# Performance work log

Hardware: AMD Instinct MI355X
Metric: run time of the kernel (lower is better)

The kernel has to match this reference:

```python
import jax, jax.numpy as jnp
import numpy as np

# Lens/CCD constants from the source module
DX = 0.00859375
F = 8.0
OX = 5.5 / 2.0   # CCD_width / 2
OY = 7.7 / 2.0   # CCD_length / 2

B, C, H, W = 4, 3, 1024, 2048


def _make_bn(h, w):
    # bn[i, j] = floor((cos(atan(dx*(j-ox)/f)) - 1) * (i - oy)), as in __init__
    j = np.arange(w, dtype=np.float64)
    i = np.arange(h, dtype=np.float64)
    a0 = np.arctan(DX * (j - OX) / F)
    bn = np.floor((np.cos(a0)[None, :] - 1.0) * (i[:, None] - OY))
    return bn.astype(np.int32)


def setup_inputs() -> dict:
    key = jax.random.key(0)
    k1, k2 = jax.random.split(key)
    x = jax.random.normal(k1, (B, C, H, W), dtype=jnp.float32)
    # Conv2d(3, 3, kernel_size=3, bias=False) weight: (out_c, in_c, kh, kw)
    weight = jax.random.normal(k2, (3, 3, 3, 3), dtype=jnp.float32) * 0.1
    bn = jnp.asarray(_make_bn(H, W))  # int32 distortion LUT, shape (H, W)
    return {"x": x, "weight": weight, "bn": bn}


def reference(x, weight, bn):
    B_, C_, H_, W_ = x.shape
    Hi, Wj = H_ - 2, W_ // 2 - 2  # active region: i+2 < H and j+2 < W//2
    i = jnp.arange(Hi)
    j = jnp.arange(Wj)
    p = jnp.arange(3)  # k // 3 (patch row)
    q = jnp.arange(3)  # k % 3  (patch col)
    # column used for the LUT wraps for j >= 256 (j1 = j % 256)
    j1 = jnp.where(j >= 256, j % 256, j)
    rows = i[:, None] + p[None, :]        # (Hi, 3)
    cols = j1[:, None] + q[None, :]       # (Wj, 3)
    # tb(i, j, p, q) = i + p + bn[i + p, j1 + q]
    bn_sel = bn[rows[:, None, :, None], cols[None, :, None, :]]  # (Hi, Wj, 3, 3)
    R = rows[:, None, :, None] + bn_sel                          # source row indices
    # Faithful quirk from the source: patch column index into input is q (0..2),
    # NOT j + q: matrix1[:, :, p, q] = input[:, :, tb, q]
    gathered = x[:, :, R, q]  # (B, C, Hi, Wj, 3, 3)
    out_act = jnp.einsum('bcijpq,ocpq->boij', gathered, weight)  # per-pixel 3x3 conv
    # guard from the source: only write when i + 2 + bn[i+2, j+2] < H
    mask = (i[:, None] + 2 + bn[i[:, None] + 2, j[None, :] + 2]) < H_
    out_act = out_act * mask.astype(out_act.dtype)
    return jnp.zeros((B_, C_, H_, W_), x.dtype).at[:, :, :Hi, :Wj].set(out_act)
```

## Files before the change

### kernel.cpp

```cpp
#include <hip/hip_runtime.h>


#define HH 1024
#define WW 2048
#define HI 1022
#define WJ 1022

#define VWS_FLOATS (12 * 1024 * 256)

__global__ __launch_bounds__(256) void compute_v_kernel(
    const float* __restrict__ x,
    const float* __restrict__ w,
    const int*   __restrict__ bn,
    float*       __restrict__ ws)
{
    const int i  = blockIdx.x;
    const int jm = threadIdx.x;

    int Rv[3][3];
    #pragma unroll
    for (int p = 0; p < 3; ++p) {
        const int r = i + p;
        const int* bnrow = bn + (size_t)r * WW;
        #pragma unroll
        for (int q = 0; q < 3; ++q) {
            int rv = r + bnrow[jm + q];
            if (rv < 0) rv += HH;
            Rv[p][q] = rv;
        }
    }

    float acc[4][3];
    #pragma unroll
    for (int b = 0; b < 4; ++b)
        #pragma unroll
        for (int o = 0; o < 3; ++o)
            acc[b][o] = 0.f;

    #pragma unroll
    for (int b = 0; b < 4; ++b) {
        #pragma unroll
        for (int c = 0; c < 3; ++c) {
            const float* xbase = x + (size_t)(b * 3 + c) * (HH * WW);
            #pragma unroll
            for (int p = 0; p < 3; ++p) {
                #pragma unroll
                for (int q = 0; q < 3; ++q) {
                    const float xv = xbase[(size_t)Rv[p][q] * WW + q];
                    #pragma unroll
                    for (int o = 0; o < 3; ++o)
                        acc[b][o] += xv * w[(o * 3 + c) * 9 + p * 3 + q];
                }
            }
        }
    }

    #pragma unroll
    for (int b = 0; b < 4; ++b)
        #pragma unroll
        for (int o = 0; o < 3; ++o)
            ws[((size_t)(b * 3 + o) * HH + i) * 256 + jm] = acc[b][o];

    float* mws = ws + VWS_FLOATS;
    const int* bnm = bn + (size_t)(i + 2) * WW;
    #pragma unroll
    for (int k = 0; k < 4; ++k) {
        const int j = jm + 256 * k;
        float m = 0.f;
        if (j < WJ)
            m = ((i + 2) + bnm[j + 2] < HH) ? 1.f : 0.f;
        mws[(size_t)i * 1024 + j] = m;
    }
}

__global__ __launch_bounds__(256) void write_kernel(
    const float* __restrict__ ws,
    float*       __restrict__ out)
{
    const int bi = blockIdx.x;
    const int b  = bi >> 10;
    const int i  = bi & 1023;
    const int j4 = threadIdx.x * 4;

    const float4 z = make_float4(0.f, 0.f, 0.f, 0.f);

    if (i < HI) {
        const float* mrow = ws + VWS_FLOATS + (size_t)i * 1024;
        const float4 mm = *(const float4*)&mrow[j4];
        #pragma unroll
        for (int o = 0; o < 3; ++o) {
            const float* vrow = ws + ((size_t)(b * 3 + o) * HH + i) * 256;
            const float4 vv = *(const float4*)&vrow[j4 & 255];
            float* orow = out + ((size_t)(b * 3 + o) * HH + i) * WW;
            *(float4*)&orow[j4] = make_float4(vv.x * mm.x, vv.y * mm.y,
                                              vv.z * mm.z, vv.w * mm.w);
            *(float4*)&orow[j4 + 1024] = z;
        }
    } else {
        #pragma unroll
        for (int o = 0; o < 3; ++o) {
            float* orow = out + ((size_t)(b * 3 + o) * HH + i) * WW;
            *(float4*)&orow[j4]        = z;
            *(float4*)&orow[j4 + 1024] = z;
        }
    }
}

extern "C" void kernel_launch(void* const* d_in, const int* in_sizes, int n_in,
                              void* d_out, int out_size, void* d_ws, size_t ws_size,
                              hipStream_t stream) {
    const float* x   = (const float*)d_in[0];
    const float* w   = (const float*)d_in[1];
    const int*   bn  = (const int*)d_in[2];
    float*       out = (float*)d_out;
    float*       ws  = (float*)d_ws;

    compute_v_kernel<<<dim3(HI), dim3(256), 0, stream>>>(x, w, bn, ws);
    write_kernel<<<dim3(4096), dim3(256), 0, stream>>>(ws, out);
}
```

Before: 190.4 us.

## Fuse compute and write kernels into one kernel staging values in shared memory

Merges the two-kernel pipeline into a single kernel where each block computes its row's 256 per-column conv values and mask into shared memory, then writes the full output row for all batches and channels directly. This removes the global workspace round-trip and one kernel launch. Each block now does more serial work (12 row stores) and only 1024 blocks are launched instead of 1022 plus 4096, which may reduce store parallelism.

Result: faster. 183.4 us (-3.7%).

```diff
diff --git a/kernel.cpp b/kernel.cpp
--- a/kernel.cpp
+++ b/kernel.cpp
@@ -6,29 +6,19 @@
 #define HI 1022
 #define WJ 1022
 
-#define VWS_FLOATS (12 * 1024 * 256)
-
-__global__ __launch_bounds__(256) void compute_v_kernel(
+__global__ __launch_bounds__(256) void dis_conv_kernel(
     const float* __restrict__ x,
     const float* __restrict__ w,
     const int*   __restrict__ bn,
-    float*       __restrict__ ws)
+    float*       __restrict__ out)
 {
-    const int i  = blockIdx.x;
-    const int jm = threadIdx.x;
+    const int i = blockIdx.x;
+    const int t = threadIdx.x;
 
-    int Rv[3][3];
-    #pragma unroll
-    for (int p = 0; p < 3; ++p) {
-        const int r = i + p;
-        const int* bnrow = bn + (size_t)r * WW;
-        #pragma unroll
-        for (int q = 0; q < 3; ++q) {
-            int rv = r + bnrow[jm + q];
-            if (rv < 0) rv += HH;
-            Rv[p][q] = rv;
-        }
-    }
+    __shared__ __align__(16) float v[12][256];
+    __shared__ __align__(16) float mask_s[1024];
+
+    const bool activeRow = (i < HI);
 
     float acc[4][3];
     #pragma unroll
@@ -37,72 +27,62 @@
         for (int o = 0; o < 3; ++o)
             acc[b][o] = 0.f;
 
-    #pragma unroll
-    for (int b = 0; b < 4; ++b) {
+    if (activeRow) {
+        int Rv[3][3];
         #pragma unroll
-        for (int c = 0; c < 3; ++c) {
-            const float* xbase = x + (size_t)(b * 3 + c) * (HH * WW);
+        for (int p = 0; p < 3; ++p) {
+            const int* bnrow = bn + (size_t)(i + p) * WW;
             #pragma unroll
-            for (int p = 0; p < 3; ++p) {
+            for (int q = 0; q < 3; ++q) {
+                int rv = i + p + bnrow[t + q];
+                if (rv < 0) rv += HH;
+                Rv[p][q] = rv;
+            }
+        }
+        #pragma unroll
+        for (int b = 0; b < 4; ++b) {
+            #pragma unroll
+            for (int c = 0; c < 3; ++c) {
+                const float* xbase = x + (size_t)(b * 3 + c) * (HH * WW);
                 #pragma unroll
-                for (int q = 0; q < 3; ++q) {
-                    const float xv = xbase[(size_t)Rv[p][q] * WW + q];
+                for (int p = 0; p < 3; ++p) {
                     #pragma unroll
-                    for (int o = 0; o < 3; ++o)
-                        acc[b][o] += xv * w[(o * 3 + c) * 9 + p * 3 + q];
+                    for (int q = 0; q < 3; ++q) {
+                        const float xv = xbase[(size_t)Rv[p][q] * WW + q];
+                        #pragma unroll
+                        for (int o = 0; o < 3; ++o)
+                            acc[b][o] += xv * w[(o * 3 + c) * 9 + p * 3 + q];
+                    }
                 }
             }
         }
     }
-
     #pragma unroll
     for (int b = 0; b < 4; ++b)
         #pragma unroll
         for (int o = 0; o < 3; ++o)
-            ws[((size_t)(b * 3 + o) * HH + i) * 256 + jm] = acc[b][o];
+            v[b * 3 + o][t] = acc[b][o];
 
-    float* mws = ws + VWS_FLOATS;
-    const int* bnm = bn + (size_t)(i + 2) * WW;
     #pragma unroll
     for (int k = 0; k < 4; ++k) {
-        const int j = jm + 256 * k;
+        const int j = t + 256 * k;
         float m = 0.f;
-        if (j < WJ)
-            m = ((i + 2) + bnm[j + 2] < HH) ? 1.f : 0.f;
-        mws[(size_t)i * 1024 + j] = m;
+        if (activeRow && j < WJ)
+            m = ((i + 2) + bn[(size_t)(i + 2) * WW + (j + 2)] < HH) ? 1.f : 0.f;
+        mask_s[j] = m;
     }
-}
+    __syncthreads();
 
-__global__ __launch_bounds__(256) void write_kernel(
-    const float* __restrict__ ws,
-    float*       __restrict__ out)
-{
-    const int bi = blockIdx.x;
-    const int b  = bi >> 10;
-    const int i  = bi & 1023;
-    const int j4 = threadIdx.x * 4;
-
+    const int j4 = t * 4;
     const float4 z = make_float4(0.f, 0.f, 0.f, 0.f);
-
-    if (i < HI) {
-        const float* mrow = ws + VWS_FLOATS + (size_t)i * 1024;
-        const float4 mm = *(const float4*)&mrow[j4];
-        #pragma unroll
-        for (int o = 0; o < 3; ++o) {
-            const float* vrow = ws + ((size_t)(b * 3 + o) * HH + i) * 256;
-            const float4 vv = *(const float4*)&vrow[j4 & 255];
-            float* orow = out + ((size_t)(b * 3 + o) * HH + i) * WW;
-            *(float4*)&orow[j4] = make_float4(vv.x * mm.x, vv.y * mm.y,
-                                              vv.z * mm.z, vv.w * mm.w);
-            *(float4*)&orow[j4 + 1024] = z;
-        }
-    } else {
-        #pragma unroll
-        for (int o = 0; o < 3; ++o) {
-            float* orow = out + ((size_t)(b * 3 + o) * HH + i) * WW;
-            *(float4*)&orow[j4]        = z;
-            *(float4*)&orow[j4 + 1024] = z;
-        }
+    const float4 mm = *(const float4*)&mask_s[j4];
+    #pragma unroll
+    for (int bo = 0; bo < 12; ++bo) {
+        float* orow = out + ((size_t)bo * HH + i) * WW;
+        const float4 vv = *(const float4*)&v[bo][j4 & 255];
+        *(float4*)&orow[j4] = make_float4(vv.x * mm.x, vv.y * mm.y,
+                                          vv.z * mm.z, vv.w * mm.w);
+        *(float4*)&orow[j4 + 1024] = z;
     }
 }
 
@@ -113,8 +93,6 @@
     const float* w   = (const float*)d_in[1];
     const int*   bn  = (const int*)d_in[2];
     float*       out = (float*)d_out;
-    float*       ws  = (float*)d_ws;
 
-    compute_v_kernel<<<dim3(HI), dim3(256), 0, stream>>>(x, w, bn, ws);
-    write_kernel<<<dim3(4096), dim3(256), 0, stream>>>(ws, out);
+    dis_conv_kernel<<<dim3(1024), dim3(256), 0, stream>>>(x, w, bn, out);
 }
```
